# Kernel tuning notes

Hardware: AMD Instinct MI355X
Metric: run time of the kernel (lower is better)

The kernel has to match this reference:

```python
import jax, jax.numpy as jnp
import numpy as np

N_NODES = 50000


def gcn_conv(x, src, dst, norm, W, b):
    # x: [N, Fin] -> linear transform then normalized scatter-add aggregation
    h = x @ W  # [N, Fout]
    msg = h[src] * norm[:, None]  # [E', Fout] gather + scale
    out = jax.ops.segment_sum(msg, dst, num_segments=N_NODES)  # scatter-add
    return out + b


def _build_graph(edge_index):
    # add self-loops (PyG GCNConv default) and compute symmetric normalization
    n = N_NODES
    loops = jnp.arange(n, dtype=edge_index.dtype)
    src = jnp.concatenate([edge_index[0], loops])
    dst = jnp.concatenate([edge_index[1], loops])
    deg = jax.ops.segment_sum(jnp.ones_like(dst, dtype=jnp.float32), dst, num_segments=n)
    dinv = jnp.where(deg > 0, jax.lax.rsqrt(deg), 0.0)
    norm = dinv[src] * dinv[dst]  # [E+N]
    return src, dst, norm


def setup_inputs() -> dict:
    key = jax.random.key(0)
    ks = jax.random.split(key, 8)
    in_c, out_c = 128, 64
    hid = 2 * out_c
    n_edges = 800000
    x = jax.random.normal(ks[0], (N_NODES, in_c), dtype=jnp.float32)
    edge_index = jax.random.randint(ks[1], (2, n_edges), 0, N_NODES, dtype=jnp.int64)
    s = 1.0 / np.sqrt(in_c)
    W1 = jax.random.uniform(ks[2], (in_c, hid), minval=-s, maxval=s, dtype=jnp.float32)
    b1 = jnp.zeros((hid,), dtype=jnp.float32)
    s2 = 1.0 / np.sqrt(hid)
    W_mu = jax.random.uniform(ks[3], (hid, out_c), minval=-s2, maxval=s2, dtype=jnp.float32)
    b_mu = jnp.zeros((out_c,), dtype=jnp.float32)
    W_ls = jax.random.uniform(ks[4], (hid, out_c), minval=-s2, maxval=s2, dtype=jnp.float32)
    b_ls = jnp.zeros((out_c,), dtype=jnp.float32)
    return {"x": x, "edge_index": edge_index, "W1": W1, "b1": b1,
            "W_mu": W_mu, "b_mu": b_mu, "W_ls": W_ls, "b_ls": b_ls}


def reference(x, edge_index, W1, b1, W_mu, b_mu, W_ls, b_ls):
    src, dst, norm = _build_graph(edge_index)
    h = jax.nn.relu(gcn_conv(x, src, dst, norm, W1, b1))
    mu = gcn_conv(h, src, dst, norm, W_mu, b_mu)
    logstd = gcn_conv(h, src, dst, norm, W_ls, b_ls)
    return mu, logstd
```

## Files before the change

kernel.cpp:

```cpp
#include <hip/hip_runtime.h>

#define N_NODES 50000
#define NE      800000
#define FDIM    128
#define OUTC    64
#define CAP     64
#define NXCD    8
#define SLICE   6250
#define NCHK    391

typedef _Float16 half4 __attribute__((ext_vector_type(4)));
typedef _Float16 f16x8 __attribute__((ext_vector_type(8)));
typedef float    f32x4 __attribute__((ext_vector_type(4)));



__global__ __launch_bounds__(256) void k_prep(int4* __restrict__ deg4,
                                              const float* __restrict__ W1,
                                              const float* __restrict__ Wmu,
                                              const float* __restrict__ Wls,
                                              const float* __restrict__ bmu,
                                              const float* __restrict__ bls,
                                              _Float16* __restrict__ W1T,
                                              _Float16* __restrict__ WoT,
                                              float* __restrict__ bo) {
    int b = blockIdx.x, tid = threadIdx.x;
    if (b < 49) {
        int i = b * 256 + tid;
        if (i < 12500) deg4[i] = make_int4(0, 0, 0, 0);
    } else {
        int j = (b - 49) * 256 + tid;
        if (j < 16384) {
            int n = j >> 7, k = j & 127;
            W1T[j] = (_Float16)W1[k * 128 + n];
        } else if (j < 32768) {
            int jj = j - 16384;
            int n = jj >> 7, k = jj & 127;
            WoT[jj] = (_Float16)(n < 64 ? Wmu[k * 64 + n] : Wls[k * 64 + (n - 64)]);
        } else if (j < 32896) {
            int n = j - 32768;
            bo[n] = (n < 64) ? bmu[n] : bls[n - 64];
        }
    }
}


__global__ __launch_bounds__(256) void k_count_fill(const int* __restrict__ ei,
                                                    int* __restrict__ deg,
                                                    int* __restrict__ pks) {
    int bid = blockIdx.x;
    int k8  = bid & 7;
    int lo  = k8 * SLICE;
    int e0  = (bid >> 3) * 2048 + threadIdx.x * 8;
    if (e0 >= NE) return;
    int4 d0 = *reinterpret_cast<const int4*>(&ei[NE + e0]);
    int4 d1 = *reinterpret_cast<const int4*>(&ei[NE + e0 + 4]);
    int4 s0 = *reinterpret_cast<const int4*>(&ei[e0]);
    int4 s1 = *reinterpret_cast<const int4*>(&ei[e0 + 4]);
    int dd[8] = {d0.x, d0.y, d0.z, d0.w, d1.x, d1.y, d1.z, d1.w};
    int ss[8] = {s0.x, s0.y, s0.z, s0.w, s1.x, s1.y, s1.z, s1.w};
    #pragma unroll
    for (int j = 0; j < 8; ++j) {
        unsigned int rel = (unsigned int)(dd[j] - lo);
        if (rel < SLICE) {
            int slot = atomicAdd(&deg[dd[j]], 1);
            if (slot < CAP) pks[dd[j] * CAP + slot] = ss[j];
        }
    }
}


__global__ __launch_bounds__(256) void k_scale(const float* __restrict__ x,
                                               const int* __restrict__ deg,
                                               float* __restrict__ dinv,
                                               _Float16* __restrict__ x16) {
    int i = blockIdx.x * 256 + threadIdx.x;
    if (i >= (N_NODES * FDIM) / 4) return;
    int node = i >> 5;
    float dv = rsqrtf((float)(deg[node] + 1));
    if ((i & 31) == 0) dinv[node] = dv;
    float4 v = reinterpret_cast<const float4*>(x)[i];
    half4 h = {(_Float16)(dv * v.x), (_Float16)(dv * v.y),
               (_Float16)(dv * v.z), (_Float16)(dv * v.w)};
    reinterpret_cast<half4*>(x16)[i] = h;
}


__device__ __forceinline__ void add8h(float* a, f16x8 h) {
    #pragma unroll
    for (int j = 0; j < 8; ++j) a[j] += (float)h[j];
}

__device__ __forceinline__ void agg_tile(const _Float16* __restrict__ in,
                                         const int* __restrict__ pks,
                                         const int* __restrict__ deg,
                                         const float* __restrict__ dinv,
                                         _Float16 (*__restrict__ As)[136]) {
    int tid = threadIdx.x;
    int rl = tid >> 4;
    int r  = blockIdx.x * 16 + rl;
    int lane8 = (tid & 15) * 8;
    int cnt = deg[r]; if (cnt > CAP) cnt = CAP;
    const int* prow = pks + r * CAP;
    float a0[8] = {0,0,0,0,0,0,0,0};
    float a1[8] = {0,0,0,0,0,0,0,0};
    int e = 0;
    for (; e + 4 <= cnt; e += 4) {
        int s0 = prow[e], s1 = prow[e+1], s2 = prow[e+2], s3 = prow[e+3];
        f16x8 x0 = *reinterpret_cast<const f16x8*>(&in[(size_t)s0 * FDIM + lane8]);
        f16x8 x1 = *reinterpret_cast<const f16x8*>(&in[(size_t)s1 * FDIM + lane8]);
        f16x8 x2 = *reinterpret_cast<const f16x8*>(&in[(size_t)s2 * FDIM + lane8]);
        f16x8 x3 = *reinterpret_cast<const f16x8*>(&in[(size_t)s3 * FDIM + lane8]);
        add8h(a0, x0); add8h(a1, x1); add8h(a0, x2); add8h(a1, x3);
    }
    for (; e < cnt; ++e)
        add8h(a0, *reinterpret_cast<const f16x8*>(&in[(size_t)prow[e] * FDIM + lane8]));
    add8h(a1, *reinterpret_cast<const f16x8*>(&in[(size_t)r * FDIM + lane8]));
    float dv = dinv[r];
    f16x8 g;
    #pragma unroll
    for (int j = 0; j < 8; ++j) g[j] = (_Float16)(dv * (a0[j] + a1[j]));
    *reinterpret_cast<f16x8*>(&As[rl][lane8]) = g;
}


__global__ __launch_bounds__(256) void k_layer1(const _Float16* __restrict__ x16,
                                                const int* __restrict__ pks,
                                                const int* __restrict__ deg,
                                                const float* __restrict__ dinv,
                                                const _Float16* __restrict__ W1T,
                                                const float* __restrict__ b1,
                                                _Float16* __restrict__ H16) {
    __shared__ _Float16 As[16][136];
    agg_tile(x16, pks, deg, dinv, As);
    __syncthreads();
    int tid = threadIdx.x;
    int wave = tid >> 6, lane = tid & 63;
    int colg = lane & 15;
    int kg8 = (lane >> 4) * 8;
    f32x4 acc0 = {0.f, 0.f, 0.f, 0.f}, acc1 = {0.f, 0.f, 0.f, 0.f};
    #pragma unroll
    for (int ks = 0; ks < 4; ++ks) {
        f16x8 a  = *reinterpret_cast<const f16x8*>(&As[colg][ks * 32 + kg8]);
        f16x8 b0 = *reinterpret_cast<const f16x8*>(
            &W1T[(size_t)((2 * wave) * 16 + colg) * FDIM + ks * 32 + kg8]);
        f16x8 b1v = *reinterpret_cast<const f16x8*>(
            &W1T[(size_t)((2 * wave + 1) * 16 + colg) * FDIM + ks * 32 + kg8]);
        acc0 = __builtin_amdgcn_mfma_f32_16x16x32_f16(a, b0, acc0, 0, 0, 0);
        acc1 = __builtin_amdgcn_mfma_f32_16x16x32_f16(a, b1v, acc1, 0, 0, 0);
    }
    int r0 = (lane >> 4) * 4;
    #pragma unroll
    for (int t = 0; t < 2; ++t) {
        int col = (2 * wave + t) * 16 + colg;
        float bias = b1[col];
        f32x4 acc = t ? acc1 : acc0;
        #pragma unroll
        for (int r = 0; r < 4; ++r) {
            int m = blockIdx.x * 16 + r0 + r;
            float h = fmaxf(acc[r] + bias, 0.f);
            H16[(size_t)m * FDIM + col] = (_Float16)(dinv[m] * h);
        }
    }
}

__global__ __launch_bounds__(256) void k_layer2(const _Float16* __restrict__ h16,
                                                const int* __restrict__ pks,
                                                const int* __restrict__ deg,
                                                const float* __restrict__ dinv,
                                                const _Float16* __restrict__ WoT,
                                                const float* __restrict__ bo,
                                                float* __restrict__ MU,
                                                float* __restrict__ LS) {
    __shared__ _Float16 As[16][136];
    agg_tile(h16, pks, deg, dinv, As);
    __syncthreads();
    int tid = threadIdx.x;
    int wave = tid >> 6, lane = tid & 63;
    int colg = lane & 15;
    int kg8 = (lane >> 4) * 8;
    f32x4 acc0 = {0.f, 0.f, 0.f, 0.f}, acc1 = {0.f, 0.f, 0.f, 0.f};
    #pragma unroll
    for (int ks = 0; ks < 4; ++ks) {
        f16x8 a  = *reinterpret_cast<const f16x8*>(&As[colg][ks * 32 + kg8]);
        f16x8 b0 = *reinterpret_cast<const f16x8*>(
            &WoT[(size_t)((2 * wave) * 16 + colg) * FDIM + ks * 32 + kg8]);
        f16x8 b1v = *reinterpret_cast<const f16x8*>(
            &WoT[(size_t)((2 * wave + 1) * 16 + colg) * FDIM + ks * 32 + kg8]);
        acc0 = __builtin_amdgcn_mfma_f32_16x16x32_f16(a, b0, acc0, 0, 0, 0);
        acc1 = __builtin_amdgcn_mfma_f32_16x16x32_f16(a, b1v, acc1, 0, 0, 0);
    }
    int r0 = (lane >> 4) * 4;
    #pragma unroll
    for (int t = 0; t < 2; ++t) {
        int col = (2 * wave + t) * 16 + colg;
        float bias = bo[col];
        f32x4 acc = t ? acc1 : acc0;
        #pragma unroll
        for (int r = 0; r < 4; ++r) {
            int m = blockIdx.x * 16 + r0 + r;
            float v = acc[r] + bias;
            if (col < 64) MU[(size_t)m * OUTC + col] = v;
            else          LS[(size_t)m * OUTC + (col - 64)] = v;
        }
    }
}


extern "C" void kernel_launch(void* const* d_in, const int* in_sizes, int n_in,
                              void* d_out, int out_size, void* d_ws, size_t ws_size,
                              hipStream_t stream) {
    const float* x   = (const float*)d_in[0];
    const int*   ei  = (const int*)d_in[1];
    const float* W1  = (const float*)d_in[2];
    const float* b1  = (const float*)d_in[3];
    const float* Wmu = (const float*)d_in[4];
    const float* bmu = (const float*)d_in[5];
    const float* Wls = (const float*)d_in[6];
    const float* bls = (const float*)d_in[7];
    float* out = (float*)d_out;

    char* ws = (char*)d_ws;
    int*      deg  = (int*)     (ws + 0);
    float*    dinv = (float*)   (ws + 200000);
    int*      pks  = (int*)     (ws + 400000);
    _Float16* W1T  = (_Float16*)(ws + 13200000);
    _Float16* WoT  = (_Float16*)(ws + 13232768);
    float*    bo   = (float*)   (ws + 13265536);
    _Float16* h16  = (_Float16*)(ws + 13266048);

    _Float16* x16 = (_Float16*)d_out;

    k_prep      <<<49 + 129, 256, 0, stream>>>((int4*)deg, W1, Wmu, Wls, bmu, bls,
                                               W1T, WoT, bo);
    k_count_fill<<<NXCD * NCHK, 256, 0, stream>>>(ei, deg, pks);
    k_scale     <<<(N_NODES * FDIM / 4 + 255) / 256, 256, 0, stream>>>(x, deg, dinv, x16);

    k_layer1<<<N_NODES / 16, 256, 0, stream>>>(x16, pks, deg, dinv, W1T, b1, h16);
    k_layer2<<<N_NODES / 16, 256, 0, stream>>>(h16, pks, deg, dinv, WoT, bo,
                                               out, out + (size_t)N_NODES * OUTC);
}
```

Before: 142.5 us.

## Bucket edges by destination slice before filling per-node neighbor lists

New measurement: 146.9 us. 1.03x slower.

```diff
diff --git a/kernel.cpp b/kernel.cpp
--- a/kernel.cpp
+++ b/kernel.cpp
@@ -7,7 +7,8 @@
 #define CAP     64
 #define NXCD    8
 #define SLICE   6250
-#define NCHK    391
+#define QCAP    131072
+#define NFB     391
 
 typedef _Float16 half4 __attribute__((ext_vector_type(4)));
 typedef _Float16 f16x8 __attribute__((ext_vector_type(8)));
@@ -27,7 +28,7 @@
     int b = blockIdx.x, tid = threadIdx.x;
     if (b < 49) {
         int i = b * 256 + tid;
-        if (i < 12500) deg4[i] = make_int4(0, 0, 0, 0);
+        if (i < 12502) deg4[i] = make_int4(0, 0, 0, 0);
     } else {
         int j = (b - 49) * 256 + tid;
         if (j < 16384) {
@@ -45,27 +46,72 @@
 }
 
 
-__global__ __launch_bounds__(256) void k_count_fill(const int* __restrict__ ei,
-                                                    int* __restrict__ deg,
-                                                    int* __restrict__ pks) {
-    int bid = blockIdx.x;
-    int k8  = bid & 7;
-    int lo  = k8 * SLICE;
-    int e0  = (bid >> 3) * 2048 + threadIdx.x * 8;
-    if (e0 >= NE) return;
-    int4 d0 = *reinterpret_cast<const int4*>(&ei[NE + e0]);
-    int4 d1 = *reinterpret_cast<const int4*>(&ei[NE + e0 + 4]);
-    int4 s0 = *reinterpret_cast<const int4*>(&ei[e0]);
-    int4 s1 = *reinterpret_cast<const int4*>(&ei[e0 + 4]);
-    int dd[8] = {d0.x, d0.y, d0.z, d0.w, d1.x, d1.y, d1.z, d1.w};
-    int ss[8] = {s0.x, s0.y, s0.z, s0.w, s1.x, s1.y, s1.z, s1.w};
-    #pragma unroll
-    for (int j = 0; j < 8; ++j) {
-        unsigned int rel = (unsigned int)(dd[j] - lo);
-        if (rel < SLICE) {
-            int slot = atomicAdd(&deg[dd[j]], 1);
-            if (slot < CAP) pks[dd[j] * CAP + slot] = ss[j];
-        }
+__global__ __launch_bounds__(256) void k_qbin(const int* __restrict__ ei,
+                                              int* __restrict__ gCur,
+                                              int* __restrict__ q) {
+    __shared__ int binCnt[8], binOff[9], binBase[8];
+    __shared__ int packed[2048];
+    int tid = threadIdx.x;
+    if (tid < 8) binCnt[tid] = 0;
+    __syncthreads();
+    int e0 = blockIdx.x * 2048 + tid * 8;
+    int myBin[8], myPos[8], myPk[8];
+    bool have = (e0 < NE);
+    if (have) {
+        int4 d0 = *reinterpret_cast<const int4*>(&ei[NE + e0]);
+        int4 d1 = *reinterpret_cast<const int4*>(&ei[NE + e0 + 4]);
+        int4 s0 = *reinterpret_cast<const int4*>(&ei[e0]);
+        int4 s1 = *reinterpret_cast<const int4*>(&ei[e0 + 4]);
+        int dd[8] = {d0.x, d0.y, d0.z, d0.w, d1.x, d1.y, d1.z, d1.w};
+        int ss[8] = {s0.x, s0.y, s0.z, s0.w, s1.x, s1.y, s1.z, s1.w};
+        #pragma unroll
+        for (int j = 0; j < 8; ++j) {
+            int b = dd[j] / SLICE;
+            myBin[j] = b;
+            myPos[j] = atomicAdd(&binCnt[b], 1);
+            myPk[j]  = ((dd[j] - b * SLICE) << 16) | ss[j];
+        }
+    }
+    __syncthreads();
+    if (tid == 0) {
+        int acc = 0;
+        #pragma unroll
+        for (int b = 0; b < 8; ++b) { binOff[b] = acc; acc += binCnt[b]; }
+        binOff[8] = acc;
+    }
+    __syncthreads();
+    if (tid < 8) binBase[tid] = atomicAdd(&gCur[tid], binCnt[tid]);
+    __syncthreads();
+    if (have) {
+        #pragma unroll
+        for (int j = 0; j < 8; ++j)
+            packed[binOff[myBin[j]] + myPos[j]] = myPk[j];
+    }
+    __syncthreads();
+    int total = binOff[8];
+    for (int i = tid; i < total; i += 256) {
+        int b = 7;
+        #pragma unroll
+        for (int t = 6; t >= 0; --t) if (i < binOff[t + 1]) b = t;
+        q[b * QCAP + binBase[b] + (i - binOff[b])] = packed[i];
+    }
+}
+
+
+__global__ __launch_bounds__(256) void k_fill2(const int* __restrict__ q,
+                                               const int* __restrict__ gCur,
+                                               int* __restrict__ deg,
+                                               int* __restrict__ pks) {
+    int k8 = blockIdx.x & 7;
+    int idx = (blockIdx.x >> 3) * 256 + threadIdx.x;
+    int n = gCur[k8];
+    int lo = k8 * SLICE;
+    for (int i = idx; i < n; i += NFB * 256) {
+        int p = q[k8 * QCAP + i];
+        int s = p & 0xFFFF;
+        int d = lo + (p >> 16);
+        int slot = atomicAdd(&deg[d], 1);
+        if (slot < CAP) pks[d * CAP + slot] = s;
     }
 }
 
@@ -222,19 +268,22 @@
 
     char* ws = (char*)d_ws;
     int*      deg  = (int*)     (ws + 0);
-    float*    dinv = (float*)   (ws + 200000);
-    int*      pks  = (int*)     (ws + 400000);
-    _Float16* W1T  = (_Float16*)(ws + 13200000);
-    _Float16* WoT  = (_Float16*)(ws + 13232768);
-    float*    bo   = (float*)   (ws + 13265536);
-    _Float16* h16  = (_Float16*)(ws + 13266048);
+    int*      gCur = (int*)     (ws + 200000);
+    float*    dinv = (float*)   (ws + 200064);
+    int*      pks  = (int*)     (ws + 400128);
+    _Float16* W1T  = (_Float16*)(ws + 13200128);
+    _Float16* WoT  = (_Float16*)(ws + 13232896);
+    float*    bo   = (float*)   (ws + 13265664);
+    int*      q    = (int*)     (ws + 13266432);
+    _Float16* h16  = (_Float16*)(ws + 17460736);
 
     _Float16* x16 = (_Float16*)d_out;
 
-    k_prep      <<<49 + 129, 256, 0, stream>>>((int4*)deg, W1, Wmu, Wls, bmu, bls,
-                                               W1T, WoT, bo);
-    k_count_fill<<<NXCD * NCHK, 256, 0, stream>>>(ei, deg, pks);
-    k_scale     <<<(N_NODES * FDIM / 4 + 255) / 256, 256, 0, stream>>>(x, deg, dinv, x16);
+    k_prep <<<49 + 129, 256, 0, stream>>>((int4*)deg, W1, Wmu, Wls, bmu, bls,
+                                          W1T, WoT, bo);
+    k_qbin <<<(NE + 2047) / 2048, 256, 0, stream>>>(ei, gCur, q);
+    k_fill2<<<NXCD * NFB, 256, 0, stream>>>(q, gCur, deg, pks);
+    k_scale<<<(N_NODES * FDIM / 4 + 255) / 256, 256, 0, stream>>>(x, deg, dinv, x16);
 
     k_layer1<<<N_NODES / 16, 256, 0, stream>>>(x16, pks, deg, dinv, W1T, b1, h16);
     k_layer2<<<N_NODES / 16, 256, 0, stream>>>(h16, pks, deg, dinv, WoT, bo,
```
